# Kernel tuning notes

Measured on AMD Instinct MI355X. Metric: run time of the kernel, lower is better.

The kernel has to match this reference:

```python
import jax, jax.numpy as jnp
import numpy as np

B, N, S = 64, 256, 2000
BETA = 0.95
K = int(round(S * (1.0 - BETA)))  # = 100, exact top-k CVaR reformulation
BIL = 4
SAFETY = 0.5
T_DF = 5.0
JITTER = 1e-4  # CHOLESKY_JITTER
N_ITERS = 200


def setup_inputs() -> dict:
    key = jax.random.key(0)
    k1, k2, k3 = jax.random.split(key, 3)
    mu = 0.01 * jax.random.normal(k1, (B, N), dtype=jnp.float32)
    # PSD covariance: sigma = A A^T / N
    A = 0.02 * jax.random.normal(k2, (B, N, N), dtype=jnp.float32)
    sigma = jnp.einsum('bij,bkj->bik', A, A) / N
    # standardized Student-T noise (matches _sample_noise with df>2)
    eps = jax.random.t(k3, T_DF, (B, S, N)) / jnp.sqrt(T_DF / (T_DF - 2.0))
    return {'mu': mu, 'sigma': sigma, 'eps': eps.astype(jnp.float32),
            'is_crisis': 1, 'lambda_risk': 0}


def _simplex_proj(v, z):
    # Euclidean projection of each row of v onto {x >= 0, sum(x) = z}
    n = v.shape[-1]
    u = jnp.flip(jnp.sort(v, axis=-1), axis=-1)          # descending
    css = jnp.cumsum(u, axis=-1) - z
    ind = jnp.arange(1, n + 1, dtype=v.dtype)
    rho = jnp.sum((u - css / ind) > 0, axis=-1)           # (B,) >= 1
    theta = jnp.take_along_axis(css, rho[:, None] - 1, axis=-1) / rho[:, None].astype(v.dtype)
    return jnp.maximum(v - theta, 0.0)


def _solve_cvar(R, floor):
    # minimize CVaR_beta(-R w) = mean of top-K scenario losses,
    # s.t. sum(w)=1, w>=0, w[BIL] >= floor[BIL]  (projected subgradient)
    b, n = R.shape[0], R.shape[2]
    mass = 1.0 - floor.sum()

    def proj(w):
        return _simplex_proj(w - floor, mass) + floor

    w0 = proj(jnp.full((b, n), 1.0 / n, dtype=R.dtype))

    def step(w, t):
        losses = -jnp.einsum('bsn,bn->bs', R, w)          # (B,S)
        thresh = jax.lax.top_k(losses, K)[0][:, -1:]      # K-th largest loss
        m = (losses >= thresh).astype(R.dtype)
        m = m / jnp.maximum(m.sum(-1, keepdims=True), float(K))
        g = -jnp.einsum('bs,bsn->bn', m, R)               # subgradient of top-K mean
        lr = 0.5 / jnp.sqrt(t + 1.0)
        return proj(w - lr * g), None

    w, _ = jax.lax.scan(step, w0, jnp.arange(N_ITERS, dtype=R.dtype))
    return w


def reference(mu, sigma, eps, is_crisis, lambda_risk):
    # 1) Cholesky reparameterization sampling: R = mu + eps @ L^T
    L = jnp.linalg.cholesky(sigma + JITTER * jnp.eye(N, dtype=sigma.dtype))
    R = mu[:, None, :] + jnp.einsum('bsn,bmn->bsm', eps, L)  # (B,S,N)
    if lambda_risk > 0:
        R = R + mu[:, None, :] / max(float(lambda_risk), 0.1)
    # 2) safety floor on BIL when in crisis
    floor = jnp.zeros((N,), dtype=mu.dtype).at[BIL].set(SAFETY * float(is_crisis))
    # 3) batched CVaR solve
    w = _solve_cvar(R, floor)
    # 4) post clamp + renormalize (as in the torch forward)
    w = jnp.maximum(w, 0.0)
    return w / (w.sum(-1, keepdims=True) + 1e-8)
```

## Files before the change

### kernel.cpp

```cpp
#include <hip/hip_runtime.h>
#include <stdint.h>

#define B_   64
#define N_   256
#define S_   2000
#define K_   100
#define BIL_ 4
#define NITER_ 200
#define JITTER_ 1e-4f
#define SAFETY_ 0.5f
#define PART_ 4
#define SCH_  (S_ / PART_)

#define OFF_LC16  ((size_t)0)
#define OFF_LR16  (OFF_LC16 + (size_t)B_ * N_ * N_ / 2)
#define OFF_EPST  (OFF_LR16 + (size_t)B_ * N_ * N_ / 2)
#define OFF_EPSRM (OFF_EPST + (size_t)B_ * N_ * S_ / 2)
#define OFF_LOSS  (OFF_EPSRM + (size_t)B_ * S_ * N_ / 2)
#define OFF_BAR   (OFF_LOSS + (size_t)2 * B_ * S_)

__device__ __forceinline__ float wred_f(float x) {
#pragma unroll
  for (int off = 32; off > 0; off >>= 1) x += __shfl_xor(x, off);
  return x;
}
__device__ __forceinline__ int wred_i(int x) {
#pragma unroll
  for (int off = 32; off > 0; off >>= 1) x += __shfl_xor(x, off);
  return x;
}
__device__ __forceinline__ unsigned keyd(float x) {
  unsigned u = __float_as_uint(x);
  unsigned ku = (u & 0x80000000u) ? ~u : (u | 0x80000000u);
  return ~ku;
}
__device__ __forceinline__ uint16_t f2b(float f) {
  uint32_t u = __float_as_uint(f);
  uint32_t r = u + 0x7FFFu + ((u >> 16) & 1u);
  return (uint16_t)(r >> 16);
}
__device__ __forceinline__ float blo(uint32_t u) { return __uint_as_float(u << 16); }
__device__ __forceinline__ float bhi(uint32_t u) { return __uint_as_float(u & 0xFFFF0000u); }

__device__ __forceinline__ float michelot4(const float vp[4], float z) {
  bool act[4] = {true, true, true, true};
  float theta = 0.0f;
  int prev = -1;
  for (int pass = 0; pass < 300; ++pass) {
    float ls = 0.0f; int lc = 0;
#pragma unroll
    for (int j = 0; j < 4; ++j) { if (act[j]) { ls += vp[j]; lc += 1; } }
    ls = wred_f(ls);
    lc = wred_i(lc);
    theta = (ls - z) / (float)lc;
    if (lc == prev) break;
    prev = lc;
#pragma unroll
    for (int j = 0; j < 4; ++j) act[j] = (vp[j] > theta);
  }
  return theta;
}

__device__ __forceinline__ void proj_store(const float y[4], float fl_bil, float mass, float muf,
                                           const float* __restrict__ muB, int ln,
                                           float* w_s, float* c_sh) {
  float vp[4];
#pragma unroll
  for (int j = 0; j < 4; ++j) {
    const int n = 4 * ln + j;
    vp[j] = y[j] - ((n == BIL_) ? fl_bil : 0.0f);
  }
  const float theta = michelot4(vp, mass);
  const float4 m4 = *(const float4*)(muB + 4 * ln);
  const float mm[4] = {m4.x, m4.y, m4.z, m4.w};
  float wj[4];
  float cp = 0.0f;
#pragma unroll
  for (int j = 0; j < 4; ++j) {
    const int n = 4 * ln + j;
    wj[j] = fmaxf(vp[j] - theta, 0.0f) + ((n == BIL_) ? fl_bil : 0.0f);
    cp = fmaf(muf * mm[j], wj[j], cp);
  }
  cp = wred_f(cp);
  if (ln == 0) *c_sh = cp;
  *(float4*)(w_s + 4 * ln) = make_float4(wj[0], wj[1], wj[2], wj[3]);
}

__global__ __launch_bounds__(512) void chol_kernel(const float* __restrict__ sigma,
                                                   float* __restrict__ Lc) {
  const int b = blockIdx.x;
  const int tid = threadIdx.x;
  const int i = tid & 255;
  const int half = tid >> 8;
  const float* Sg = sigma + (size_t)b * N_ * N_;
  float* L = Lc + (size_t)b * N_ * N_;
  __shared__ __align__(16) float slab[248 * 8];
  __shared__ __align__(16) float spart[256][8];
  __shared__ __align__(16) float pnl[64];

  for (int j0 = 0; j0 < N_; j0 += 8) {
    for (int x = tid; x < j0 * 8; x += 512) {
      const int k = x >> 3, jj = x & 7;
      slab[x] = L[(size_t)k * N_ + (j0 + jj)];
    }
    float s[8];
    if (half == 0) {
#pragma unroll
      for (int jj = 0; jj < 8; ++jj) {
        float a = Sg[(size_t)(j0 + jj) * N_ + i];
        if (i == j0 + jj) a += JITTER_;
        s[jj] = a;
      }
    } else {
#pragma unroll
      for (int jj = 0; jj < 8; ++jj) s[jj] = 0.0f;
    }
    __syncthreads();

    const int kb = half ? (j0 >> 1) : 0;
    const int ke = half ? j0 : (j0 >> 1);
#pragma unroll 4
    for (int k = kb; k < ke; ++k) {
      const float lk = L[(size_t)k * N_ + i];
      const float4 h0 = *(const float4*)&slab[k * 8];
      const float4 h1 = *(const float4*)&slab[k * 8 + 4];
      s[0] = fmaf(-lk, h0.x, s[0]);
      s[1] = fmaf(-lk, h0.y, s[1]);
      s[2] = fmaf(-lk, h0.z, s[2]);
      s[3] = fmaf(-lk, h0.w, s[3]);
      s[4] = fmaf(-lk, h1.x, s[4]);
      s[5] = fmaf(-lk, h1.y, s[5]);
      s[6] = fmaf(-lk, h1.z, s[6]);
      s[7] = fmaf(-lk, h1.w, s[7]);
    }
    if (half == 1) {
      *(float4*)&spart[i][0] = make_float4(s[0], s[1], s[2], s[3]);
      *(float4*)&spart[i][4] = make_float4(s[4], s[5], s[6], s[7]);
    }
    __syncthreads();

    if (half == 0) {
      const float4 p0 = *(const float4*)&spart[i][0];
      const float4 p1 = *(const float4*)&spart[i][4];
      s[0] += p0.x; s[1] += p0.y; s[2] += p0.z; s[3] += p0.w;
      s[4] += p1.x; s[5] += p1.y; s[6] += p1.z; s[7] += p1.w;
      if ((i >> 3) == (j0 >> 3)) {
        const int base = j0 & 63;
        const int r = i & 7;
        float l[8], di[8];
#pragma unroll
        for (int m = 0; m < 8; ++m) {
          const float smv = __shfl(s[m], base + m);
          const float d = sqrtf(smv);
          const float dinv = 1.0f / d;
          di[m] = dinv;
          float lm;
          if (r == m) lm = d;
          else if (r > m) lm = s[m] * dinv;
          else lm = 0.0f;
          l[m] = lm;
#pragma unroll
          for (int mm = m + 1; mm < 8; ++mm) {
            s[mm] = fmaf(-lm, __shfl(lm, base + mm), s[mm]);
          }
        }
#pragma unroll
        for (int m = 0; m < 8; ++m) pnl[r * 8 + m] = (m < r) ? l[m] : ((m == r) ? di[r] : 0.0f);
#pragma unroll
        for (int m = 0; m < 8; ++m) L[(size_t)(j0 + m) * N_ + i] = l[m];
      }
    }
    __syncthreads();

    if (half == 0 && (i >> 3) != (j0 >> 3)) {
      float l[8];
      if (i > j0) {
#pragma unroll
        for (int m = 0; m < 8; ++m) {
          float sm = s[m];
#pragma unroll
          for (int mm = 0; mm < 8; ++mm) {
            if (mm < m) sm = fmaf(-l[mm], pnl[m * 8 + mm], sm);
          }
          l[m] = sm * pnl[m * 8 + m];
        }
      } else {
#pragma unroll
        for (int m = 0; m < 8; ++m) l[m] = 0.0f;
      }
#pragma unroll
      for (int m = 0; m < 8; ++m) L[(size_t)(j0 + m) * N_ + i] = l[m];
    }
    __syncthreads();
  }
}

__global__ __launch_bounds__(256) void lpack_kernel(const float* __restrict__ Lc,
                                                    uint16_t* __restrict__ Lc16,
                                                    uint16_t* __restrict__ Lr16) {
  const int b = blockIdx.x;
  const float* Lp = Lc + (size_t)b * N_ * N_;
  uint16_t* C16 = Lc16 + (size_t)b * N_ * N_;
  uint16_t* R16 = Lr16 + (size_t)b * N_ * N_;
  __shared__ float tl[32][33];
  const int tx = threadIdx.x & 31;
  const int ty = threadIdx.x >> 5;
  for (int kt = 0; kt < 8; ++kt) {
    for (int it = 0; it < 8; ++it) {
#pragma unroll
      for (int rr = 0; rr < 4; ++rr) {
        const int k = kt * 32 + ty + 8 * rr;
        const int ii = it * 32 + tx;
        const float v = Lp[(size_t)k * N_ + ii];
        tl[ty + 8 * rr][tx] = v;
        C16[(size_t)k * N_ + ii] = f2b(v);
      }
      __syncthreads();
#pragma unroll
      for (int rr = 0; rr < 4; ++rr) {
        const int ii = it * 32 + ty + 8 * rr;
        const int k = kt * 32 + tx;
        R16[(size_t)ii * N_ + k] = f2b(tl[tx][ty + 8 * rr]);
      }
      __syncthreads();
    }
  }
}

__global__ __launch_bounds__(256) void etrans_kernel(const float* __restrict__ eps,
                                                     uint16_t* __restrict__ epsT16,
                                                     uint16_t* __restrict__ epsrm16,
                                                     int* __restrict__ bar) {
  const int b = blockIdx.x;
  const int s0 = blockIdx.y * 50;
  const int t = threadIdx.x;
  if (blockIdx.x == 0 && blockIdx.y == 0 && t < 64) bar[t] = 0;
  __shared__ float tl[50][257];
  const float* E = eps + ((size_t)b * S_ + s0) * N_;
  for (int p = 0; p < 50; ++p) tl[p][t] = E[(size_t)p * N_ + t];
  __syncthreads();
  uint16_t* RM = epsrm16 + ((size_t)b * S_ + s0) * N_;
  for (int p = 0; p < 50; ++p) RM[(size_t)p * N_ + t] = f2b(tl[p][t]);
  uint16_t* ET = epsT16 + (size_t)b * N_ * S_;
  const int g = t / 50, ss = t % 50;
  if (g < 5) {
    for (int q = 0; q < 52; ++q) {
      const int n = q * 5 + g;
      if (n < N_) ET[(size_t)n * S_ + s0 + ss] = f2b(tl[ss][n]);
    }
  }
}

__global__ __launch_bounds__(1024) void solve_kernel(
    const float* __restrict__ mu, const int* __restrict__ pcrisis,
    const int* __restrict__ plam, const uint16_t* __restrict__ Lc16,
    const uint16_t* __restrict__ Lr16, const uint16_t* __restrict__ epsT16,
    const uint16_t* __restrict__ epsrm16, unsigned* __restrict__ lossbits,
    int* __restrict__ bar, float* __restrict__ out) {
  const int bx = blockIdx.x;
  const int b = bx & (B_ - 1);
  const int part = bx >> 6;
  const int t = threadIdx.x;
  const int ln = t & 63;
  const int s0 = part * SCH_;

  __shared__ __align__(16) float w_s[N_];
  __shared__ __align__(16) float v_s[N_];
  __shared__ __align__(16) float scratch[8][N_];
  __shared__ __align__(16) uint16_t lists[S_];
  __shared__ __align__(16) int hist[4][256];
  __shared__ float c_sh;
  __shared__ int lcnt;
  __shared__ float sum_sh;

  const int crisis = pcrisis[0];
  const int lamv = plam[0];
  const float muf = 1.0f + ((lamv > 0) ? (1.0f / fmaxf((float)lamv, 0.1f)) : 0.0f);
  const float fl_bil = SAFETY_ * (float)crisis;
  const float mass = 1.0f - fl_bil;

  const uint16_t* LcB = Lc16 + (size_t)b * N_ * N_;
  const uint16_t* LrB = Lr16 + (size_t)b * N_ * N_;
  const float* muB = mu + (size_t)b * N_;
  const uint16_t* epsTB = epsT16 + (size_t)b * N_ * S_;
  const uint16_t* epsRB = epsrm16 + (size_t)b * S_ * N_;
  float* sc1 = &scratch[0][0];

  if (t < 64) {
    float y[4];
#pragma unroll
    for (int j = 0; j < 4; ++j) y[j] = 1.0f / (float)N_;
    proj_store(y, fl_bil, mass, muf, muB, ln, w_s, &c_sh);
  }
  __syncthreads();

  for (int it = 0; it < NITER_; ++it) {
    {
      const int oct = t >> 7, kp = t & 127;
      const uint32_t* Lp = (const uint32_t*)(LrB) + kp;
      const int i0 = 32 * oct;
      float a0 = 0.0f, a1 = 0.0f;
#pragma unroll 8
      for (int ii = 0; ii < 32; ++ii) {
        const uint32_t u = Lp[(size_t)(i0 + ii) * (N_ / 2)];
        const float ww = w_s[i0 + ii];
        a0 = fmaf(blo(u), ww, a0);
        a1 = fmaf(bhi(u), ww, a1);
      }
      *(float2*)&scratch[oct][2 * kp] = make_float2(a0, a1);
    }
    __syncthreads();

    if (t < N_) {
      v_s[t] = ((scratch[0][t] + scratch[1][t]) + (scratch[2][t] + scratch[3][t])) +
               ((scratch[4][t] + scratch[5][t]) + (scratch[6][t] + scratch[7][t]));
    } else {
      for (int x = t - 256; x < 4 * 256; x += 768) ((int*)hist)[x] = 0;
      if (t == 256) lcnt = 0;
    }
    __syncthreads();

    const float cc = c_sh;
    {
      const int q = t >> 8;
      const int idx = t & 255;
      if (idx < SCH_ / 2) {
        const uint32_t* col = (const uint32_t*)(epsTB + (size_t)(64 * q) * S_) + (s0 / 2 + idx);
        float a0 = 0.0f, a1 = 0.0f;
#pragma unroll 8
        for (int j = 0; j < 64; ++j) {
          const uint32_t u = col[(size_t)j * (S_ / 2)];
          const float vv = v_s[64 * q + j];
          a0 = fmaf(blo(u), vv, a0);
          a1 = fmaf(bhi(u), vv, a1);
        }
        *(float2*)&sc1[q * SCH_ + 2 * idx] = make_float2(a0, a1);
      }
    }
    __syncthreads();

    unsigned* lgbuf = lossbits + ((it & 1) ? (size_t)B_ * S_ : 0) + (size_t)b * S_;
    if (t < SCH_) {
      const float lv = -(cc + ((sc1[t] + sc1[SCH_ + t]) + (sc1[2 * SCH_ + t] + sc1[3 * SCH_ + t])));
      __hip_atomic_store(&lgbuf[s0 + t], keyd(lv), __ATOMIC_RELAXED, __HIP_MEMORY_SCOPE_AGENT);
    }
    __syncthreads();

    if (t == 0) {
      __hip_atomic_fetch_add(&bar[b], 1, __ATOMIC_RELAXED, __HIP_MEMORY_SCOPE_AGENT);
      const int target = PART_ * (it + 1);
      while (__hip_atomic_load(&bar[b], __ATOMIC_RELAXED, __HIP_MEMORY_SCOPE_AGENT) < target) {
        __builtin_amdgcn_s_sleep(1);
      }
    }
    __syncthreads();

    uint32_t kx = 0xFFFFFFFFu, ky = 0xFFFFFFFFu;
    if (t < S_ / 2) {
      const unsigned long long two = __hip_atomic_load(
          (const unsigned long long*)(lgbuf + 2 * t), __ATOMIC_RELAXED, __HIP_MEMORY_SCOPE_AGENT);
      kx = (uint32_t)two;
      ky = (uint32_t)(two >> 32);
      atomicAdd(&hist[0][kx >> 24], 1);
      atomicAdd(&hist[0][ky >> 24], 1);
    }
    __syncthreads();

    unsigned pref = 0;
    int r = K_;
#pragma unroll
    for (int pass = 0; pass < 4; ++pass) {
      const int shift = 24 - 8 * pass;
      {
        const int4 c4 = *(const int4*)&hist[pass][4 * ln];
        const int c0 = c4.x, c1 = c4.y, c2 = c4.z, c3 = c4.w;
        const int tot = c0 + c1 + c2 + c3;
        int sc = tot;
#pragma unroll
        for (int off = 1; off < 64; off <<= 1) {
          const int o = __shfl_up(sc, off);
          if (ln >= off) sc += o;
        }
        const int excl = sc - tot;
        const bool has = (excl < r) && (r <= sc);
        const unsigned long long bal = __ballot(has);
        const int lstar = __ffsll(bal) - 1;
        const int bc0 = __shfl(c0, lstar);
        const int bc1 = __shfl(c1, lstar);
        const int bc2 = __shfl(c2, lstar);
        const int bexcl = __shfl(excl, lstar);
        const int rr = r - bexcl;
        int d, rn;
        if (rr <= bc0) { d = 0; rn = rr; }
        else if (rr <= bc0 + bc1) { d = 1; rn = rr - bc0; }
        else if (rr <= bc0 + bc1 + bc2) { d = 2; rn = rr - bc0 - bc1; }
        else { d = 3; rn = rr - bc0 - bc1 - bc2; }
        pref |= (unsigned)(4 * lstar + d) << shift;
        r = rn;
      }
      if (pass < 3) {
        const unsigned msk = 0xFFFFFFFFu << shift;
        const int nshift = shift - 8;
        if (t < S_ / 2) {
          if ((kx & msk) == pref) atomicAdd(&hist[pass + 1][(kx >> nshift) & 255], 1);
          if ((ky & msk) == pref) atomicAdd(&hist[pass + 1][(ky >> nshift) & 255], 1);
        }
      } else {
        if (t < S_ / 2) {
          if (kx <= pref) { const int p = atomicAdd(&lcnt, 1); lists[p] = (uint16_t)(2 * t); }
          if (ky <= pref) { const int p = atomicAdd(&lcnt, 1); lists[p] = (uint16_t)(2 * t + 1); }
        }
      }
      __syncthreads();
    }

    const int cnt = lcnt;
    const float weight = 1.0f / (float)((cnt > K_) ? cnt : K_);

    {
      const int rt = t >> 7;
      const int np = t & 127;
      float a0 = 0.0f, a1 = 0.0f;
      for (int p = rt; p < cnt; p += 8) {
        const uint32_t u = *((const uint32_t*)(epsRB + (size_t)lists[p] * N_) + np);
        a0 += blo(u);
        a1 += bhi(u);
      }
      *(float2*)&scratch[rt][2 * np] = make_float2(a0, a1);
    }
    __syncthreads();

    if (t < 64) {
      float4 acc = make_float4(0.0f, 0.0f, 0.0f, 0.0f);
#pragma unroll
      for (int oct = 0; oct < 8; ++oct) {
        const float4 x = *(const float4*)&scratch[oct][4 * ln];
        acc.x += x.x; acc.y += x.y; acc.z += x.z; acc.w += x.w;
      }
      *(float4*)&v_s[4 * ln] = acc;
    }
    __syncthreads();

    {
      const int oct = t >> 7, ip = t & 127;
      const uint32_t* Lp = (const uint32_t*)(LcB) + ip;
      const int k0 = 32 * oct;
      float a0 = 0.0f, a1 = 0.0f;
#pragma unroll 8
      for (int kk = 0; kk < 32; ++kk) {
        const uint32_t u = Lp[(size_t)(k0 + kk) * (N_ / 2)];
        const float ee = v_s[k0 + kk];
        a0 = fmaf(blo(u), ee, a0);
        a1 = fmaf(bhi(u), ee, a1);
      }
      *(float2*)&scratch[oct][2 * ip] = make_float2(a0, a1);
    }
    __syncthreads();

    if (t < 64) {
      float4 u4 = make_float4(0.0f, 0.0f, 0.0f, 0.0f);
#pragma unroll
      for (int oct = 0; oct < 8; ++oct) {
        const float4 x = *(const float4*)&scratch[oct][4 * ln];
        u4.x += x.x; u4.y += x.y; u4.z += x.z; u4.w += x.w;
      }
      const float lr = 0.5f / sqrtf((float)it + 1.0f);
      const float4 w4 = *(const float4*)(w_s + 4 * ln);
      const float4 m4 = *(const float4*)(muB + 4 * ln);
      float y[4];
      y[0] = w4.x + lr * (muf * m4.x + u4.x * weight);
      y[1] = w4.y + lr * (muf * m4.y + u4.y * weight);
      y[2] = w4.z + lr * (muf * m4.z + u4.z * weight);
      y[3] = w4.w + lr * (muf * m4.w + u4.w * weight);
      proj_store(y, fl_bil, mass, muf, muB, ln, w_s, &c_sh);
    }
    __syncthreads();
  }

  if (part == 0) {
    if (t < 64) {
      const float4 w4 = *(const float4*)(w_s + 4 * ln);
      const float ssum = wred_f(w4.x + w4.y + w4.z + w4.w);
      if (ln == 0) sum_sh = ssum;
    }
    __syncthreads();
    if (t < N_) out[(size_t)b * N_ + t] = fmaxf(w_s[t], 0.0f) / (sum_sh + 1e-8f);
  }
}

extern "C" void kernel_launch(void* const* d_in, const int* in_sizes, int n_in,
                              void* d_out, int out_size, void* d_ws, size_t ws_size,
                              hipStream_t stream) {
  const float* mu = (const float*)d_in[0];
  const float* sigma = (const float*)d_in[1];
  const float* eps = (const float*)d_in[2];
  const int* crisis = (const int*)d_in[3];
  const int* lam = (const int*)d_in[4];
  float* out = (float*)d_out;
  float* ws = (float*)d_ws;

  uint16_t* Lc16 = (uint16_t*)(ws + OFF_LC16);
  uint16_t* Lr16 = (uint16_t*)(ws + OFF_LR16);
  uint16_t* epsT16 = (uint16_t*)(ws + OFF_EPST);
  uint16_t* epsrm16 = (uint16_t*)(ws + OFF_EPSRM);
  float* Lc = ws + OFF_EPSRM;
  unsigned* lossbits = (unsigned*)(ws + OFF_LOSS);
  int* bar = (int*)(ws + OFF_BAR);

  chol_kernel<<<dim3(B_), dim3(512), 0, stream>>>(sigma, Lc);
  lpack_kernel<<<dim3(B_), dim3(256), 0, stream>>>(Lc, Lc16, Lr16);
  etrans_kernel<<<dim3(B_, S_ / 50), dim3(256), 0, stream>>>(eps, epsT16, epsrm16, bar);

  solve_kernel<<<dim3(PART_ * B_), dim3(1024), 0, stream>>>(
      mu, crisis, lam, Lc16, Lr16, epsT16, epsrm16, lossbits, bar, out);
}
```

Before: 4.230 ms.

## Restructure CVaR solve iterations into wave-reduced matvecs with warm-started projection

The two L matvecs change from column-strided partial sums followed by a block reduction into per-wave row dot products reduced with shuffles. This removes two barrier stages per iteration. The simplex projection now warm-starts Michelot from the previous theta and counts active entries with ballots. The first-level histogram for the local partition is built before the cross-block barrier, and the top-K gather is unrolled by two. The warm start risks converging to a different theta if the previous one overshoots, and the shuffle-heavy matvecs add cross-lane work.

```diff
diff --git a/kernel.cpp b/kernel.cpp
--- a/kernel.cpp
+++ b/kernel.cpp
@@ -24,11 +24,6 @@
   for (int off = 32; off > 0; off >>= 1) x += __shfl_xor(x, off);
   return x;
 }
-__device__ __forceinline__ int wred_i(int x) {
-#pragma unroll
-  for (int off = 32; off > 0; off >>= 1) x += __shfl_xor(x, off);
-  return x;
-}
 __device__ __forceinline__ unsigned keyd(float x) {
   unsigned u = __float_as_uint(x);
   unsigned ku = (u & 0x80000000u) ? ~u : (u | 0x80000000u);
@@ -42,35 +37,42 @@
 __device__ __forceinline__ float blo(uint32_t u) { return __uint_as_float(u << 16); }
 __device__ __forceinline__ float bhi(uint32_t u) { return __uint_as_float(u & 0xFFFF0000u); }
 
-__device__ __forceinline__ float michelot4(const float vp[4], float z) {
-  bool act[4] = {true, true, true, true};
-  float theta = 0.0f;
+__device__ __forceinline__ float michelot4(const float vp[4], float z, float theta0) {
+  float theta = theta0;
   int prev = -1;
   for (int pass = 0; pass < 300; ++pass) {
-    float ls = 0.0f; int lc = 0;
-#pragma unroll
-    for (int j = 0; j < 4; ++j) { if (act[j]) { ls += vp[j]; lc += 1; } }
+    const bool a0 = vp[0] > theta, a1 = vp[1] > theta, a2 = vp[2] > theta, a3 = vp[3] > theta;
+    float ls = 0.0f;
+    if (a0) ls += vp[0];
+    if (a1) ls += vp[1];
+    if (a2) ls += vp[2];
+    if (a3) ls += vp[3];
+    const int lc = __popcll(__ballot(a0)) + __popcll(__ballot(a1)) +
+                   __popcll(__ballot(a2)) + __popcll(__ballot(a3));
     ls = wred_f(ls);
-    lc = wred_i(lc);
-    theta = (ls - z) / (float)lc;
+    if (lc == 0) {
+      theta = -1e30f;
+      prev = -1;
+      continue;
+    }
+    const float nt = (ls - z) / (float)lc;
+    theta = nt;
     if (lc == prev) break;
     prev = lc;
-#pragma unroll
-    for (int j = 0; j < 4; ++j) act[j] = (vp[j] > theta);
   }
   return theta;
 }
 
 __device__ __forceinline__ void proj_store(const float y[4], float fl_bil, float mass, float muf,
-                                           const float* __restrict__ muB, int ln,
-                                           float* w_s, float* c_sh) {
+                                           const float* __restrict__ muB, int ln, float theta0,
+                                           float* w_s, float* c_sh, float* th_sh) {
   float vp[4];
 #pragma unroll
   for (int j = 0; j < 4; ++j) {
     const int n = 4 * ln + j;
     vp[j] = y[j] - ((n == BIL_) ? fl_bil : 0.0f);
   }
-  const float theta = michelot4(vp, mass);
+  const float theta = michelot4(vp, mass, theta0);
   const float4 m4 = *(const float4*)(muB + 4 * ln);
   const float mm[4] = {m4.x, m4.y, m4.z, m4.w};
   float wj[4];
@@ -82,7 +84,10 @@
     cp = fmaf(muf * mm[j], wj[j], cp);
   }
   cp = wred_f(cp);
-  if (ln == 0) *c_sh = cp;
+  if (ln == 0) {
+    *c_sh = cp;
+    *th_sh = theta;
+  }
   *(float4*)(w_s + 4 * ln) = make_float4(wj[0], wj[1], wj[2], wj[3]);
 }
 
@@ -262,14 +267,17 @@
   const int part = bx >> 6;
   const int t = threadIdx.x;
   const int ln = t & 63;
+  const int wv = t >> 6;
   const int s0 = part * SCH_;
 
   __shared__ __align__(16) float w_s[N_];
   __shared__ __align__(16) float v_s[N_];
+  __shared__ __align__(16) float u_s[N_];
   __shared__ __align__(16) float scratch[8][N_];
   __shared__ __align__(16) uint16_t lists[S_];
   __shared__ __align__(16) int hist[4][256];
   __shared__ float c_sh;
+  __shared__ float th_sh;
   __shared__ int lcnt;
   __shared__ float sum_sh;
 
@@ -290,33 +298,25 @@
     float y[4];
 #pragma unroll
     for (int j = 0; j < 4; ++j) y[j] = 1.0f / (float)N_;
-    proj_store(y, fl_bil, mass, muf, muB, ln, w_s, &c_sh);
+    proj_store(y, fl_bil, mass, muf, muB, ln, -1e30f, w_s, &c_sh, &th_sh);
   }
   __syncthreads();
 
   for (int it = 0; it < NITER_; ++it) {
     {
-      const int oct = t >> 7, kp = t & 127;
-      const uint32_t* Lp = (const uint32_t*)(LrB) + kp;
-      const int i0 = 32 * oct;
-      float a0 = 0.0f, a1 = 0.0f;
-#pragma unroll 8
-      for (int ii = 0; ii < 32; ++ii) {
-        const uint32_t u = Lp[(size_t)(i0 + ii) * (N_ / 2)];
-        const float ww = w_s[i0 + ii];
-        a0 = fmaf(blo(u), ww, a0);
-        a1 = fmaf(bhi(u), ww, a1);
-      }
-      *(float2*)&scratch[oct][2 * kp] = make_float2(a0, a1);
-    }
-    __syncthreads();
-
-    if (t < N_) {
-      v_s[t] = ((scratch[0][t] + scratch[1][t]) + (scratch[2][t] + scratch[3][t])) +
-               ((scratch[4][t] + scratch[5][t]) + (scratch[6][t] + scratch[7][t]));
-    } else {
-      for (int x = t - 256; x < 4 * 256; x += 768) ((int*)hist)[x] = 0;
-      if (t == 256) lcnt = 0;
+      ((int*)hist)[t] = 0;
+      if (t == 0) lcnt = 0;
+      const float4 w4 = *(const float4*)(w_s + 4 * ln);
+      float vk = 0.0f;
+#pragma unroll
+      for (int j = 0; j < 16; ++j) {
+        const int k = 16 * wv + j;
+        const uint2 u2 = ((const uint2*)(LcB + (size_t)k * N_))[ln];
+        float a = blo(u2.x) * w4.x + bhi(u2.x) * w4.y + blo(u2.y) * w4.z + bhi(u2.y) * w4.w;
+        a = wred_f(a);
+        if (ln == j) vk = a;
+      }
+      if (ln < 16) v_s[16 * wv + ln] = vk;
     }
     __syncthreads();
 
@@ -342,7 +342,9 @@
     unsigned* lgbuf = lossbits + ((it & 1) ? (size_t)B_ * S_ : 0) + (size_t)b * S_;
     if (t < SCH_) {
       const float lv = -(cc + ((sc1[t] + sc1[SCH_ + t]) + (sc1[2 * SCH_ + t] + sc1[3 * SCH_ + t])));
-      __hip_atomic_store(&lgbuf[s0 + t], keyd(lv), __ATOMIC_RELAXED, __HIP_MEMORY_SCOPE_AGENT);
+      const unsigned kd = keyd(lv);
+      __hip_atomic_store(&lgbuf[s0 + t], kd, __ATOMIC_RELAXED, __HIP_MEMORY_SCOPE_AGENT);
+      atomicAdd(&hist[0][kd >> 24], 1);
     }
     __syncthreads();
 
@@ -361,8 +363,10 @@
           (const unsigned long long*)(lgbuf + 2 * t), __ATOMIC_RELAXED, __HIP_MEMORY_SCOPE_AGENT);
       kx = (uint32_t)two;
       ky = (uint32_t)(two >> 32);
-      atomicAdd(&hist[0][kx >> 24], 1);
-      atomicAdd(&hist[0][ky >> 24], 1);
+      if ((unsigned)(2 * t - s0) >= (unsigned)SCH_) {
+        atomicAdd(&hist[0][kx >> 24], 1);
+        atomicAdd(&hist[0][ky >> 24], 1);
+      }
     }
     __syncthreads();
 
@@ -420,59 +424,54 @@
     {
       const int rt = t >> 7;
       const int np = t & 127;
-      float a0 = 0.0f, a1 = 0.0f;
-      for (int p = rt; p < cnt; p += 8) {
+      float a0 = 0.0f, a1 = 0.0f, b0 = 0.0f, b1 = 0.0f;
+      for (int p = rt; p < cnt; p += 16) {
         const uint32_t u = *((const uint32_t*)(epsRB + (size_t)lists[p] * N_) + np);
         a0 += blo(u);
         a1 += bhi(u);
-      }
-      *(float2*)&scratch[rt][2 * np] = make_float2(a0, a1);
+        const int p2 = p + 8;
+        if (p2 < cnt) {
+          const uint32_t u2 = *((const uint32_t*)(epsRB + (size_t)lists[p2] * N_) + np);
+          b0 += blo(u2);
+          b1 += bhi(u2);
+        }
+      }
+      *(float2*)&scratch[rt][2 * np] = make_float2(a0 + b0, a1 + b1);
+    }
+    __syncthreads();
+
+    {
+      float4 e4 = make_float4(0.0f, 0.0f, 0.0f, 0.0f);
+#pragma unroll
+      for (int g = 0; g < 8; ++g) {
+        const float4 x = *(const float4*)&scratch[g][4 * ln];
+        e4.x += x.x; e4.y += x.y; e4.z += x.z; e4.w += x.w;
+      }
+      float ui = 0.0f;
+#pragma unroll
+      for (int j = 0; j < 16; ++j) {
+        const int i = 16 * wv + j;
+        const uint2 u2 = ((const uint2*)(LrB + (size_t)i * N_))[ln];
+        float a = blo(u2.x) * e4.x + bhi(u2.x) * e4.y + blo(u2.y) * e4.z + bhi(u2.y) * e4.w;
+        a = wred_f(a);
+        if (ln == j) ui = a;
+      }
+      if (ln < 16) u_s[16 * wv + ln] = ui;
     }
     __syncthreads();
 
     if (t < 64) {
-      float4 acc = make_float4(0.0f, 0.0f, 0.0f, 0.0f);
-#pragma unroll
-      for (int oct = 0; oct < 8; ++oct) {
-        const float4 x = *(const float4*)&scratch[oct][4 * ln];
-        acc.x += x.x; acc.y += x.y; acc.z += x.z; acc.w += x.w;
-      }
-      *(float4*)&v_s[4 * ln] = acc;
-    }
-    __syncthreads();
-
-    {
-      const int oct = t >> 7, ip = t & 127;
-      const uint32_t* Lp = (const uint32_t*)(LcB) + ip;
-      const int k0 = 32 * oct;
-      float a0 = 0.0f, a1 = 0.0f;
-#pragma unroll 8
-      for (int kk = 0; kk < 32; ++kk) {
-        const uint32_t u = Lp[(size_t)(k0 + kk) * (N_ / 2)];
-        const float ee = v_s[k0 + kk];
-        a0 = fmaf(blo(u), ee, a0);
-        a1 = fmaf(bhi(u), ee, a1);
-      }
-      *(float2*)&scratch[oct][2 * ip] = make_float2(a0, a1);
-    }
-    __syncthreads();
-
-    if (t < 64) {
-      float4 u4 = make_float4(0.0f, 0.0f, 0.0f, 0.0f);
-#pragma unroll
-      for (int oct = 0; oct < 8; ++oct) {
-        const float4 x = *(const float4*)&scratch[oct][4 * ln];
-        u4.x += x.x; u4.y += x.y; u4.z += x.z; u4.w += x.w;
-      }
+      const float th0 = th_sh;
       const float lr = 0.5f / sqrtf((float)it + 1.0f);
       const float4 w4 = *(const float4*)(w_s + 4 * ln);
+      const float4 u4 = *(const float4*)(u_s + 4 * ln);
       const float4 m4 = *(const float4*)(muB + 4 * ln);
       float y[4];
       y[0] = w4.x + lr * (muf * m4.x + u4.x * weight);
       y[1] = w4.y + lr * (muf * m4.y + u4.y * weight);
       y[2] = w4.z + lr * (muf * m4.z + u4.z * weight);
       y[3] = w4.w + lr * (muf * m4.w + u4.w * weight);
-      proj_store(y, fl_bil, mass, muf, muB, ln, w_s, &c_sh);
+      proj_store(y, fl_bil, mass, muf, muB, ln, th0, w_s, &c_sh, &th_sh);
     }
     __syncthreads();
   }
```

Result: slower. 8.997 ms (+112.7%).

## Warm-start simplex projection, build local histogram early, and unroll gather loop

Applied to the files above, without the earlier changes.

The Michelot simplex projection now starts from the previous iteration's threshold and counts active entries with ballot/popcount instead of an integer shuffle reduction, which should cut the number of passes and per-pass cost. The first radix-histogram pass now adds each block's own loss keys before the cross-block barrier and skips them afterwards, moving some atomics off the critical path after the spin-wait. The top-K row gather loop is unrolled by two with independent accumulators to raise memory-level parallelism. A warm start that overshoots can leave no active entries, so the code falls back to a reset when the count is zero.

```diff
diff --git a/kernel.cpp b/kernel.cpp
--- a/kernel.cpp
+++ b/kernel.cpp
@@ -24,11 +24,6 @@
   for (int off = 32; off > 0; off >>= 1) x += __shfl_xor(x, off);
   return x;
 }
-__device__ __forceinline__ int wred_i(int x) {
-#pragma unroll
-  for (int off = 32; off > 0; off >>= 1) x += __shfl_xor(x, off);
-  return x;
-}
 __device__ __forceinline__ unsigned keyd(float x) {
   unsigned u = __float_as_uint(x);
   unsigned ku = (u & 0x80000000u) ? ~u : (u | 0x80000000u);
@@ -42,35 +37,41 @@
 __device__ __forceinline__ float blo(uint32_t u) { return __uint_as_float(u << 16); }
 __device__ __forceinline__ float bhi(uint32_t u) { return __uint_as_float(u & 0xFFFF0000u); }
 
-__device__ __forceinline__ float michelot4(const float vp[4], float z) {
-  bool act[4] = {true, true, true, true};
-  float theta = 0.0f;
+__device__ __forceinline__ float michelot4(const float vp[4], float z, float theta0) {
+  float theta = theta0;
   int prev = -1;
   for (int pass = 0; pass < 300; ++pass) {
-    float ls = 0.0f; int lc = 0;
-#pragma unroll
-    for (int j = 0; j < 4; ++j) { if (act[j]) { ls += vp[j]; lc += 1; } }
+    const bool a0 = vp[0] > theta, a1 = vp[1] > theta, a2 = vp[2] > theta, a3 = vp[3] > theta;
+    float ls = 0.0f;
+    if (a0) ls += vp[0];
+    if (a1) ls += vp[1];
+    if (a2) ls += vp[2];
+    if (a3) ls += vp[3];
+    const int lc = __popcll(__ballot(a0)) + __popcll(__ballot(a1)) +
+                   __popcll(__ballot(a2)) + __popcll(__ballot(a3));
     ls = wred_f(ls);
-    lc = wred_i(lc);
+    if (lc == 0) {
+      theta = -1e30f;
+      prev = -1;
+      continue;
+    }
     theta = (ls - z) / (float)lc;
     if (lc == prev) break;
     prev = lc;
-#pragma unroll
-    for (int j = 0; j < 4; ++j) act[j] = (vp[j] > theta);
   }
   return theta;
 }
 
 __device__ __forceinline__ void proj_store(const float y[4], float fl_bil, float mass, float muf,
-                                           const float* __restrict__ muB, int ln,
-                                           float* w_s, float* c_sh) {
+                                           const float* __restrict__ muB, int ln, float theta0,
+                                           float* w_s, float* c_sh, float* th_sh) {
   float vp[4];
 #pragma unroll
   for (int j = 0; j < 4; ++j) {
     const int n = 4 * ln + j;
     vp[j] = y[j] - ((n == BIL_) ? fl_bil : 0.0f);
   }
-  const float theta = michelot4(vp, mass);
+  const float theta = michelot4(vp, mass, theta0);
   const float4 m4 = *(const float4*)(muB + 4 * ln);
   const float mm[4] = {m4.x, m4.y, m4.z, m4.w};
   float wj[4];
@@ -82,7 +83,10 @@
     cp = fmaf(muf * mm[j], wj[j], cp);
   }
   cp = wred_f(cp);
-  if (ln == 0) *c_sh = cp;
+  if (ln == 0) {
+    *c_sh = cp;
+    *th_sh = theta;
+  }
   *(float4*)(w_s + 4 * ln) = make_float4(wj[0], wj[1], wj[2], wj[3]);
 }
 
@@ -270,6 +274,7 @@
   __shared__ __align__(16) uint16_t lists[S_];
   __shared__ __align__(16) int hist[4][256];
   __shared__ float c_sh;
+  __shared__ float th_sh;
   __shared__ int lcnt;
   __shared__ float sum_sh;
 
@@ -290,7 +295,7 @@
     float y[4];
 #pragma unroll
     for (int j = 0; j < 4; ++j) y[j] = 1.0f / (float)N_;
-    proj_store(y, fl_bil, mass, muf, muB, ln, w_s, &c_sh);
+    proj_store(y, fl_bil, mass, muf, muB, ln, -1e30f, w_s, &c_sh, &th_sh);
   }
   __syncthreads();
 
@@ -342,7 +347,9 @@
     unsigned* lgbuf = lossbits + ((it & 1) ? (size_t)B_ * S_ : 0) + (size_t)b * S_;
     if (t < SCH_) {
       const float lv = -(cc + ((sc1[t] + sc1[SCH_ + t]) + (sc1[2 * SCH_ + t] + sc1[3 * SCH_ + t])));
-      __hip_atomic_store(&lgbuf[s0 + t], keyd(lv), __ATOMIC_RELAXED, __HIP_MEMORY_SCOPE_AGENT);
+      const unsigned kd = keyd(lv);
+      __hip_atomic_store(&lgbuf[s0 + t], kd, __ATOMIC_RELAXED, __HIP_MEMORY_SCOPE_AGENT);
+      atomicAdd(&hist[0][kd >> 24], 1);
     }
     __syncthreads();
 
@@ -361,8 +368,10 @@
           (const unsigned long long*)(lgbuf + 2 * t), __ATOMIC_RELAXED, __HIP_MEMORY_SCOPE_AGENT);
       kx = (uint32_t)two;
       ky = (uint32_t)(two >> 32);
-      atomicAdd(&hist[0][kx >> 24], 1);
-      atomicAdd(&hist[0][ky >> 24], 1);
+      if ((unsigned)(2 * t - s0) >= (unsigned)SCH_) {
+        atomicAdd(&hist[0][kx >> 24], 1);
+        atomicAdd(&hist[0][ky >> 24], 1);
+      }
     }
     __syncthreads();
 
@@ -420,13 +429,19 @@
     {
       const int rt = t >> 7;
       const int np = t & 127;
-      float a0 = 0.0f, a1 = 0.0f;
-      for (int p = rt; p < cnt; p += 8) {
+      float a0 = 0.0f, a1 = 0.0f, b0 = 0.0f, b1 = 0.0f;
+      for (int p = rt; p < cnt; p += 16) {
         const uint32_t u = *((const uint32_t*)(epsRB + (size_t)lists[p] * N_) + np);
         a0 += blo(u);
         a1 += bhi(u);
-      }
-      *(float2*)&scratch[rt][2 * np] = make_float2(a0, a1);
+        const int p2 = p + 8;
+        if (p2 < cnt) {
+          const uint32_t u2 = *((const uint32_t*)(epsRB + (size_t)lists[p2] * N_) + np);
+          b0 += blo(u2);
+          b1 += bhi(u2);
+        }
+      }
+      *(float2*)&scratch[rt][2 * np] = make_float2(a0 + b0, a1 + b1);
     }
     __syncthreads();
 
@@ -458,6 +473,7 @@
     __syncthreads();
 
     if (t < 64) {
+      const float th0 = th_sh;
       float4 u4 = make_float4(0.0f, 0.0f, 0.0f, 0.0f);
 #pragma unroll
       for (int oct = 0; oct < 8; ++oct) {
@@ -472,7 +488,7 @@
       y[1] = w4.y + lr * (muf * m4.y + u4.y * weight);
       y[2] = w4.z + lr * (muf * m4.z + u4.z * weight);
       y[3] = w4.w + lr * (muf * m4.w + u4.w * weight);
-      proj_store(y, fl_bil, mass, muf, muB, ln, w_s, &c_sh);
+      proj_store(y, fl_bil, mass, muf, muB, ln, th0, w_s, &c_sh, &th_sh);
     }
     __syncthreads();
   }
```

New measurement: 4.254 ms. No clear change (+0.5%).
